# Kernel optimization log

Measured on AMD Instinct MI355X. Metric: run time of the kernel, lower is better.

## Reference

```python
import jax
import jax.numpy as jnp
import numpy as np

VOCAB = 100      # len(vocab); embedding table has VOCAB+1 rows
EMBED = 10
MID = 100
SEQ = 550
OUT = 1


def setup_inputs() -> dict:
    key = jax.random.key(0)
    ks = jax.random.split(key, 8)
    s_ih = 1.0 / np.sqrt(MID)
    return {
        "x": jax.random.randint(ks[0], (SEQ,), 0, VOCAB + 1),
        "hidden": jnp.zeros((1, 1, MID), dtype=jnp.float32),
        "embed_table": jax.random.normal(ks[1], (VOCAB + 1, EMBED), dtype=jnp.float32),
        "w_ih": jax.random.uniform(ks[2], (3 * MID, EMBED), minval=-s_ih, maxval=s_ih, dtype=jnp.float32),
        "w_hh": jax.random.uniform(ks[3], (3 * MID, MID), minval=-s_ih, maxval=s_ih, dtype=jnp.float32),
        "b_ih": jax.random.uniform(ks[4], (3 * MID,), minval=-s_ih, maxval=s_ih, dtype=jnp.float32),
        "b_hh": jax.random.uniform(ks[5], (3 * MID,), minval=-s_ih, maxval=s_ih, dtype=jnp.float32),
        "fc_w": jax.random.uniform(ks[6], (OUT, MID), minval=-s_ih, maxval=s_ih, dtype=jnp.float32),
        "fc_b": jax.random.uniform(ks[7], (OUT,), minval=-s_ih, maxval=s_ih, dtype=jnp.float32),
    }


def reference(x, hidden, embed_table, w_ih, w_hh, b_ih, b_hh, fc_w, fc_b):
    # embedding lookup: [SEQ, EMBED]
    emb = embed_table[x]
    # precompute input-side gate projections for all timesteps: [SEQ, 3*MID]
    gi_all = emb @ w_ih.T + b_ih
    h0 = hidden[0, 0]  # [MID]

    def step(h, gi):
        gh = w_hh @ h + b_hh                      # [3*MID]
        i_r, i_z, i_n = jnp.split(gi, 3)
        h_r, h_z, h_n = jnp.split(gh, 3)
        r = jax.nn.sigmoid(i_r + h_r)
        z = jax.nn.sigmoid(i_z + h_z)
        n = jnp.tanh(i_n + r * h_n)
        h_new = (1.0 - z) * n + z * h
        return h_new, None

    h_final, _ = jax.lax.scan(step, h0, gi_all)   # h_final: [MID]
    out = jax.nn.sigmoid(jax.nn.relu(h_final) @ fc_w.T + fc_b)  # [OUT]
    return out.reshape(1, 1, OUT)
```

## Files before the change

kernel.cpp:

```cpp
#include <hip/hip_runtime.h>

#define SEQ 550
#define MID 100
#define TPB 256

typedef _Float16 half2_t __attribute__((ext_vector_type(2)));

union H2I { int i; half2_t h; ushort2 u2; };

__device__ __forceinline__ float fdot2(half2_t a, half2_t b, float c) {
    return __builtin_amdgcn_fdot2(a, b, c, false);
}
__device__ __forceinline__ float sigm(float x) { return 1.0f / (1.0f + __expf(-x)); }
__device__ __forceinline__ float tanh_f(float x) { return 1.0f - 2.0f / (__expf(2.0f * x) + 1.0f); }
__device__ __forceinline__ half2_t i2h(int v) { H2I u; u.i = v; return u.h; }

__device__ __forceinline__ float pair_sum(float x) {
    int yi = __builtin_amdgcn_update_dpp(0, __float_as_int(x), 0xB1, 0xF, 0xF, true);
    return x + __int_as_float(yi);
}

__global__ __launch_bounds__(TPB, 1) void gru_fused(
    const int*   __restrict__ x,
    const float* __restrict__ hidden,
    const float* __restrict__ embed,
    const float* __restrict__ w_ih,
    const float* __restrict__ w_hh,
    const float* __restrict__ b_ih,
    const float* __restrict__ b_hh,
    const float* __restrict__ fc_w,
    const float* __restrict__ fc_b,
    float*       __restrict__ out)
{
    __shared__ __align__(16) ushort seqbuf[SEQ * 16];
    __shared__ __align__(16) int hbuf[128];
    __shared__ float partial[MID];

    const int  tid = threadIdx.x;
    const bool act = tid < 2 * MID;
    const int  u   = tid >> 1;
    const int  p   = tid & 1;
    const int  hidx = (u < 50) ? u : u + 14;

    for (int i = tid; i < SEQ * 10; i += TPB) {
        int t = i / 10;
        int k = i - 10 * t;
        H2I c; c.h = half2_t{(_Float16)embed[x[t] * 10 + k], (_Float16)0.0f};
        seqbuf[t * 16 + (k < 6 ? k : k + 2)] = c.u2.x;
    }
    for (int i = tid; i < SEQ; i += TPB)
        *(int*)(seqbuf + i * 16 + 12) = 0;

    half2_t whh[3][25];
    half2_t wihr[3][3];
    float b0 = 0.f, b1 = 0.f, b2 = 0.f, b3 = 0.f;
    float hreg = 0.f, fcw = 0.f;

    if (act) {
        #pragma unroll
        for (int r = 0; r < 3; r++) {
            const int row = r * MID + u;
            const float2* wr = (const float2*)(w_hh + row * MID) + 25 * p;
            #pragma unroll
            for (int k = 0; k < 25; k++) {
                float2 f = wr[k];
                whh[r][k] = half2_t{(_Float16)f.x, (_Float16)f.y};
            }
            const float* wi = w_ih + row * 10 + 6 * p;
            wihr[r][0] = half2_t{(_Float16)wi[0], (_Float16)wi[1]};
            wihr[r][1] = half2_t{(_Float16)wi[2], (_Float16)wi[3]};
            if (p == 0) wihr[r][2] = half2_t{(_Float16)wi[4], (_Float16)wi[5]};
            else        wihr[r][2] = half2_t{(_Float16)0.0f, (_Float16)0.0f};
        }
        if (p == 0) {
            b0 = b_ih[u]           + b_hh[u];
            b1 = b_ih[MID + u]     + b_hh[MID + u];
            b2 = b_ih[2 * MID + u];
            b3 = b_hh[2 * MID + u];
        }
        hreg = hidden[u];
        fcw  = fc_w[u];
        if (p == 0) ((_Float16*)hbuf)[hidx] = (_Float16)hreg;
    }
    float fcb = (tid == 0) ? fc_b[0] : 0.0f;

    __syncthreads();

    #pragma unroll 1
    for (int t = 0; t < SEQ; t++) {
        if (act) {
            const int   rbase = ((t & 1) << 8) + (p << 7);
            const int4* hp4   = (const int4*)((const char*)hbuf + rbase);
            int4 q0 = hp4[0], q1 = hp4[1], q2 = hp4[2], q3 = hp4[3], q4 = hp4[4], q5 = hp4[5];
            int  qe = ((const int*)hp4)[24];
            int4 ev = *(const int4*)(seqbuf + t * 16 + p * 8);

            half2_t hh[25];
            hh[0]=i2h(q0.x);  hh[1]=i2h(q0.y);  hh[2]=i2h(q0.z);  hh[3]=i2h(q0.w);
            hh[4]=i2h(q1.x);  hh[5]=i2h(q1.y);  hh[6]=i2h(q1.z);  hh[7]=i2h(q1.w);
            hh[8]=i2h(q2.x);  hh[9]=i2h(q2.y);  hh[10]=i2h(q2.z); hh[11]=i2h(q2.w);
            hh[12]=i2h(q3.x); hh[13]=i2h(q3.y); hh[14]=i2h(q3.z); hh[15]=i2h(q3.w);
            hh[16]=i2h(q4.x); hh[17]=i2h(q4.y); hh[18]=i2h(q4.z); hh[19]=i2h(q4.w);
            hh[20]=i2h(q5.x); hh[21]=i2h(q5.y); hh[22]=i2h(q5.z); hh[23]=i2h(q5.w);
            hh[24]=i2h(qe);

            float s0 = b0, s1 = b1, s2 = b2, s3 = b3;
            #pragma unroll
            for (int k = 0; k < 25; k++) {
                s0 = fdot2(whh[0][k], hh[k], s0);
                s1 = fdot2(whh[1][k], hh[k], s1);
                s3 = fdot2(whh[2][k], hh[k], s3);
            }
            half2_t e0 = i2h(ev.x), e1 = i2h(ev.y), e2 = i2h(ev.z);
            s0 = fdot2(wihr[0][0], e0, s0); s0 = fdot2(wihr[0][1], e1, s0); s0 = fdot2(wihr[0][2], e2, s0);
            s1 = fdot2(wihr[1][0], e0, s1); s1 = fdot2(wihr[1][1], e1, s1); s1 = fdot2(wihr[1][2], e2, s1);
            s2 = fdot2(wihr[2][0], e0, s2); s2 = fdot2(wihr[2][1], e1, s2); s2 = fdot2(wihr[2][2], e2, s2);

            float ar  = pair_sum(s0);
            float az  = pair_sum(s1);
            float gin = pair_sum(s2);
            float ghn = pair_sum(s3);

            float r = sigm(ar);
            float z = sigm(az);
            float n = tanh_f(gin + r * ghn);
            hreg = n + z * (hreg - n);
            if (p == 0)
                ((_Float16*)hbuf)[(((t & 1) ^ 1) << 7) + hidx] = (_Float16)hreg;
        }
        __syncthreads();
    }

    if (act && p == 0) partial[u] = fmaxf(hreg, 0.0f) * fcw;
    __syncthreads();
    if (tid == 0) {
        float s = fcb;
        const float4* pp = (const float4*)partial;
        #pragma unroll
        for (int k = 0; k < 25; k++) {
            float4 f = pp[k];
            s += (f.x + f.y) + (f.z + f.w);
        }
        out[0] = sigm(s);
    }
}

extern "C" void kernel_launch(void* const* d_in, const int* in_sizes, int n_in,
                              void* d_out, int out_size, void* d_ws, size_t ws_size,
                              hipStream_t stream) {
    const int*   x      = (const int*)  d_in[0];
    const float* hidden = (const float*)d_in[1];
    const float* embed  = (const float*)d_in[2];
    const float* w_ih   = (const float*)d_in[3];
    const float* w_hh   = (const float*)d_in[4];
    const float* b_ih   = (const float*)d_in[5];
    const float* b_hh   = (const float*)d_in[6];
    const float* fc_w   = (const float*)d_in[7];
    const float* fc_b   = (const float*)d_in[8];
    float*       out    = (float*)d_out;

    gru_fused<<<1, TPB, 0, stream>>>(x, hidden, embed, w_ih, w_hh,
                                     b_ih, b_hh, fc_w, fc_b, out);
}
```

Measured before the change: 294.7 us.

## Split each GRU unit across four lanes and stage embeddings in hidden buffer

Each hidden unit is now computed by four threads instead of two, so each thread does about 15 fdot2 per gate instead of 28, and the partial sums are combined with a two-step DPP quad reduction. The embedding pair for the next step is copied into the hidden-state buffer by helper threads, so the dot-product loop reads h and x from a single contiguous LDS segment. This shortens the per-step serial dependency chain but adds another DPP stage, more waves taking part in the barrier, and extra helper writes each step.

```diff
diff --git a/kernel.cpp b/kernel.cpp
--- a/kernel.cpp
+++ b/kernel.cpp
@@ -2,7 +2,7 @@
 
 #define SEQ 550
 #define MID 100
-#define TPB 256
+#define TPB 448
 
 typedef _Float16 half2_t __attribute__((ext_vector_type(2)));
 
@@ -15,10 +15,13 @@
 __device__ __forceinline__ float tanh_f(float x) { return 1.0f - 2.0f / (__expf(2.0f * x) + 1.0f); }
 __device__ __forceinline__ half2_t i2h(int v) { H2I u; u.i = v; return u.h; }
 
-__device__ __forceinline__ float pair_sum(float x) {
-    int yi = __builtin_amdgcn_update_dpp(0, __float_as_int(x), 0xB1, 0xF, 0xF, true);
-    return x + __int_as_float(yi);
+__device__ __forceinline__ float qsum(float x) {
+    int a = __builtin_amdgcn_update_dpp(0, __float_as_int(x), 0xB1, 0xF, 0xF, true);
+    float y = x + __int_as_float(a);
+    int b = __builtin_amdgcn_update_dpp(0, __float_as_int(y), 0x4E, 0xF, 0xF, true);
+    return y + __int_as_float(b);
 }
+
 
 __global__ __launch_bounds__(TPB, 1) void gru_fused(
     const int*   __restrict__ x,
@@ -32,45 +35,52 @@
     const float* __restrict__ fc_b,
     float*       __restrict__ out)
 {
-    __shared__ __align__(16) ushort seqbuf[SEQ * 16];
-    __shared__ __align__(16) int hbuf[128];
+    __shared__ __align__(16) int   seqbuf[SEQ * 5];
+    __shared__ __align__(16) int   hbuf[128];
     __shared__ float partial[MID];
 
     const int  tid = threadIdx.x;
-    const bool act = tid < 2 * MID;
-    const int  u   = tid >> 1;
-    const int  p   = tid & 1;
-    const int  hidx = (u < 50) ? u : u + 14;
+    const bool act = tid < 4 * MID;
+    const int  u   = tid >> 2;
+    const int  p   = tid & 3;
 
-    for (int i = tid; i < SEQ * 10; i += TPB) {
-        int t = i / 10;
-        int k = i - 10 * t;
-        H2I c; c.h = half2_t{(_Float16)embed[x[t] * 10 + k], (_Float16)0.0f};
-        seqbuf[t * 16 + (k < 6 ? k : k + 2)] = c.u2.x;
+    if (tid < 128) hbuf[tid] = 0;
+    for (int i = tid; i < SEQ * 5; i += TPB) {
+        int t = i / 5, j = i - 5 * t;
+        const float* ep = embed + x[t] * 10 + 2 * j;
+        H2I c; c.h = half2_t{(_Float16)ep[0], (_Float16)ep[1]};
+        seqbuf[i] = c.i;
     }
-    for (int i = tid; i < SEQ; i += TPB)
-        *(int*)(seqbuf + i * 16 + 12) = 0;
 
-    half2_t whh[3][25];
-    half2_t wihr[3][3];
-    float b0 = 0.f, b1 = 0.f, b2 = 0.f, b3 = 0.f;
-    float hreg = 0.f, fcw = 0.f;
+    half2_t w0[15], w1[15], wn[15];
+    float b0 = 0.f, b1 = 0.f, b2 = 0.f, b3 = 0.f, hreg = 0.f, fcw = 0.f;
+    int hw_off = 0;
 
     if (act) {
+        const int segbase[4] = {0, 13, 26, 38};
+        const int segcnt[4]  = {13, 13, 12, 12};
+        const int ebase[4]   = {0, 2, 3, 4};
+        const int ecnt[4]    = {2, 1, 1, 1};
+
         #pragma unroll
         for (int r = 0; r < 3; r++) {
-            const int row = r * MID + u;
-            const float2* wr = (const float2*)(w_hh + row * MID) + 25 * p;
+            const float* WH = w_hh + (r * MID + u) * MID;
+            const float* WI = w_ih + (r * MID + u) * 10;
+            half2_t* W = (r == 0) ? w0 : (r == 1) ? w1 : wn;
             #pragma unroll
-            for (int k = 0; k < 25; k++) {
-                float2 f = wr[k];
-                whh[r][k] = half2_t{(_Float16)f.x, (_Float16)f.y};
+            for (int pos = 0; pos < 13; pos++) {
+                int m  = segbase[p] + pos;
+                int mc = m < 49 ? m : 49;
+                half2_t wv = half2_t{(_Float16)WH[2 * mc], (_Float16)WH[2 * mc + 1]};
+                W[pos] = (pos < segcnt[p]) ? wv : half2_t{(_Float16)0.f, (_Float16)0.f};
             }
-            const float* wi = w_ih + row * 10 + 6 * p;
-            wihr[r][0] = half2_t{(_Float16)wi[0], (_Float16)wi[1]};
-            wihr[r][1] = half2_t{(_Float16)wi[2], (_Float16)wi[3]};
-            if (p == 0) wihr[r][2] = half2_t{(_Float16)wi[4], (_Float16)wi[5]};
-            else        wihr[r][2] = half2_t{(_Float16)0.0f, (_Float16)0.0f};
+            #pragma unroll
+            for (int j = 0; j < 2; j++) {
+                int m  = ebase[p] + j;
+                int mc = m < 4 ? m : 4;
+                half2_t wv = half2_t{(_Float16)WI[2 * mc], (_Float16)WI[2 * mc + 1]};
+                W[13 + j] = (j < ecnt[p]) ? wv : half2_t{(_Float16)0.f, (_Float16)0.f};
+            }
         }
         if (p == 0) {
             b0 = b_ih[u]           + b_hh[u];
@@ -80,53 +90,64 @@
         }
         hreg = hidden[u];
         fcw  = fc_w[u];
-        if (p == 0) ((_Float16*)hbuf)[hidx] = (_Float16)hreg;
+        int m   = u >> 1;
+        int seg = (m < 13) ? 0 : (m < 26) ? 1 : (m < 38) ? 2 : 3;
+        hw_off  = seg * 64 + (m - segbase[seg]) * 4 + (u & 1) * 2;
     }
     float fcb = (tid == 0) ? fc_b[0] : 0.0f;
 
+    const int he = tid - 400;
+    const int my_eslot = (he == 0) ? 52 : (he == 1) ? 56 :
+                         (he == 2) ? 116 : (he == 3) ? 180 : 244;
+
     __syncthreads();
+
+    if (act && p == 0)
+        *(_Float16*)((char*)hbuf + hw_off) = (_Float16)hreg;
+    if (tid >= 400 && tid < 405)
+        *(int*)((char*)hbuf + my_eslot) = seqbuf[he];
+    __syncthreads();
+
+    const char* rdbase = (const char*)hbuf + p * 64;
 
     #pragma unroll 1
     for (int t = 0; t < SEQ; t++) {
+        const int rpar = (t & 1) << 8;
+        const int wpar = rpar ^ 256;
         if (act) {
-            const int   rbase = ((t & 1) << 8) + (p << 7);
-            const int4* hp4   = (const int4*)((const char*)hbuf + rbase);
-            int4 q0 = hp4[0], q1 = hp4[1], q2 = hp4[2], q3 = hp4[3], q4 = hp4[4], q5 = hp4[5];
-            int  qe = ((const int*)hp4)[24];
-            int4 ev = *(const int4*)(seqbuf + t * 16 + p * 8);
+            const int4* qp = (const int4*)(rdbase + rpar);
+            int4 q0 = qp[0], q1 = qp[1], q2 = qp[2], q3 = qp[3];
+            float s0 = b0, s1 = b1, s2 = b2, s3 = b3;
+            half2_t v;
+            v = i2h(q0.x); s0 = fdot2(w0[0],  v, s0); s1 = fdot2(w1[0],  v, s1); s3 = fdot2(wn[0],  v, s3);
+            v = i2h(q0.y); s0 = fdot2(w0[1],  v, s0); s1 = fdot2(w1[1],  v, s1); s3 = fdot2(wn[1],  v, s3);
+            v = i2h(q0.z); s0 = fdot2(w0[2],  v, s0); s1 = fdot2(w1[2],  v, s1); s3 = fdot2(wn[2],  v, s3);
+            v = i2h(q0.w); s0 = fdot2(w0[3],  v, s0); s1 = fdot2(w1[3],  v, s1); s3 = fdot2(wn[3],  v, s3);
+            v = i2h(q1.x); s0 = fdot2(w0[4],  v, s0); s1 = fdot2(w1[4],  v, s1); s3 = fdot2(wn[4],  v, s3);
+            v = i2h(q1.y); s0 = fdot2(w0[5],  v, s0); s1 = fdot2(w1[5],  v, s1); s3 = fdot2(wn[5],  v, s3);
+            v = i2h(q1.z); s0 = fdot2(w0[6],  v, s0); s1 = fdot2(w1[6],  v, s1); s3 = fdot2(wn[6],  v, s3);
+            v = i2h(q1.w); s0 = fdot2(w0[7],  v, s0); s1 = fdot2(w1[7],  v, s1); s3 = fdot2(wn[7],  v, s3);
+            v = i2h(q2.x); s0 = fdot2(w0[8],  v, s0); s1 = fdot2(w1[8],  v, s1); s3 = fdot2(wn[8],  v, s3);
+            v = i2h(q2.y); s0 = fdot2(w0[9],  v, s0); s1 = fdot2(w1[9],  v, s1); s3 = fdot2(wn[9],  v, s3);
+            v = i2h(q2.z); s0 = fdot2(w0[10], v, s0); s1 = fdot2(w1[10], v, s1); s3 = fdot2(wn[10], v, s3);
+            v = i2h(q2.w); s0 = fdot2(w0[11], v, s0); s1 = fdot2(w1[11], v, s1); s3 = fdot2(wn[11], v, s3);
+            v = i2h(q3.x); s0 = fdot2(w0[12], v, s0); s1 = fdot2(w1[12], v, s1); s3 = fdot2(wn[12], v, s3);
+            v = i2h(q3.y); s0 = fdot2(w0[13], v, s0); s1 = fdot2(w1[13], v, s1); s2 = fdot2(wn[13], v, s2);
+            v = i2h(q3.z); s0 = fdot2(w0[14], v, s0); s1 = fdot2(w1[14], v, s1); s2 = fdot2(wn[14], v, s2);
 
-            half2_t hh[25];
-            hh[0]=i2h(q0.x);  hh[1]=i2h(q0.y);  hh[2]=i2h(q0.z);  hh[3]=i2h(q0.w);
-            hh[4]=i2h(q1.x);  hh[5]=i2h(q1.y);  hh[6]=i2h(q1.z);  hh[7]=i2h(q1.w);
-            hh[8]=i2h(q2.x);  hh[9]=i2h(q2.y);  hh[10]=i2h(q2.z); hh[11]=i2h(q2.w);
-            hh[12]=i2h(q3.x); hh[13]=i2h(q3.y); hh[14]=i2h(q3.z); hh[15]=i2h(q3.w);
-            hh[16]=i2h(q4.x); hh[17]=i2h(q4.y); hh[18]=i2h(q4.z); hh[19]=i2h(q4.w);
-            hh[20]=i2h(q5.x); hh[21]=i2h(q5.y); hh[22]=i2h(q5.z); hh[23]=i2h(q5.w);
-            hh[24]=i2h(qe);
-
-            float s0 = b0, s1 = b1, s2 = b2, s3 = b3;
-            #pragma unroll
-            for (int k = 0; k < 25; k++) {
-                s0 = fdot2(whh[0][k], hh[k], s0);
-                s1 = fdot2(whh[1][k], hh[k], s1);
-                s3 = fdot2(whh[2][k], hh[k], s3);
-            }
-            half2_t e0 = i2h(ev.x), e1 = i2h(ev.y), e2 = i2h(ev.z);
-            s0 = fdot2(wihr[0][0], e0, s0); s0 = fdot2(wihr[0][1], e1, s0); s0 = fdot2(wihr[0][2], e2, s0);
-            s1 = fdot2(wihr[1][0], e0, s1); s1 = fdot2(wihr[1][1], e1, s1); s1 = fdot2(wihr[1][2], e2, s1);
-            s2 = fdot2(wihr[2][0], e0, s2); s2 = fdot2(wihr[2][1], e1, s2); s2 = fdot2(wihr[2][2], e2, s2);
-
-            float ar  = pair_sum(s0);
-            float az  = pair_sum(s1);
-            float gin = pair_sum(s2);
-            float ghn = pair_sum(s3);
+            float ar  = qsum(s0);
+            float az  = qsum(s1);
+            float gin = qsum(s2);
+            float ghn = qsum(s3);
 
             float r = sigm(ar);
             float z = sigm(az);
             float n = tanh_f(gin + r * ghn);
             hreg = n + z * (hreg - n);
             if (p == 0)
-                ((_Float16*)hbuf)[(((t & 1) ^ 1) << 7) + hidx] = (_Float16)hreg;
+                *(_Float16*)((char*)hbuf + wpar + hw_off) = (_Float16)hreg;
+        } else if (tid >= 400 && tid < 405 && t + 1 < SEQ) {
+            *(int*)((char*)hbuf + wpar + my_eslot) = seqbuf[(t + 1) * 5 + he];
         }
         __syncthreads();
     }
```

Result: slower. 357.4 us (+21.3%).

## Run GRU recurrence in a single wavefront using MFMA for hidden-state matvec

Applied to the files above, without the earlier changes.

Moves the recurrent w_hh·h product onto MFMA 16x16x32 f16 instructions issued by one 64-lane wavefront, with weights held as A-fragments in registers. Each lane then finishes two hidden units using fdot2 for the tail columns and input projection. The per-step block-wide __syncthreads is gone because only one wave runs the loop, leaving only intra-wave LDS exchanges. The risks are MFMA latency on the serial dependency chain, heavy register pressure, and relying on intra-wave LDS ordering with no explicit barriers.

```diff
diff --git a/kernel.cpp b/kernel.cpp
--- a/kernel.cpp
+++ b/kernel.cpp
@@ -2,11 +2,14 @@
 
 #define SEQ 550
 #define MID 100
-#define TPB 256
+#define TPB 128
 
 typedef _Float16 half2_t __attribute__((ext_vector_type(2)));
-
-union H2I { int i; half2_t h; ushort2 u2; };
+typedef _Float16 half8_t __attribute__((ext_vector_type(8)));
+typedef float f32x4 __attribute__((ext_vector_type(4)));
+
+union H2I { int i; half2_t h; };
+union H8I { int4 i4; half8_t h8; };
 
 __device__ __forceinline__ float fdot2(half2_t a, half2_t b, float c) {
     return __builtin_amdgcn_fdot2(a, b, c, false);
@@ -14,10 +17,28 @@
 __device__ __forceinline__ float sigm(float x) { return 1.0f / (1.0f + __expf(-x)); }
 __device__ __forceinline__ float tanh_f(float x) { return 1.0f - 2.0f / (__expf(2.0f * x) + 1.0f); }
 __device__ __forceinline__ half2_t i2h(int v) { H2I u; u.i = v; return u.h; }
-
-__device__ __forceinline__ float pair_sum(float x) {
-    int yi = __builtin_amdgcn_update_dpp(0, __float_as_int(x), 0xB1, 0xF, 0xF, true);
-    return x + __int_as_float(yi);
+__device__ __forceinline__ float pull_odd(float x) {
+    int y = __builtin_amdgcn_update_dpp(0, __float_as_int(x), 0xB1, 0xF, 0xF, true);
+    return __int_as_float(y);
+}
+
+template<int BASE, int CNT>
+__device__ __forceinline__ void mfma_group(const half8_t (&afr)[19][3],
+                                           half8_t b0, half8_t b1, half8_t b2,
+                                           f32x4 zf, char* gw, int m) {
+    f32x4 dd[CNT];
+    #pragma unroll
+    for (int j = 0; j < CNT; j++) {
+        f32x4 d = __builtin_amdgcn_mfma_f32_16x16x32_f16(afr[BASE + j][0], b0, zf, 0, 0, 0);
+        d = __builtin_amdgcn_mfma_f32_16x16x32_f16(afr[BASE + j][1], b1, d, 0, 0, 0);
+        d = __builtin_amdgcn_mfma_f32_16x16x32_f16(afr[BASE + j][2], b2, d, 0, 0, 0);
+        dd[j] = d;
+    }
+    if (m == 0) {
+        #pragma unroll
+        for (int j = 0; j < CNT; j++)
+            *(f32x4*)(gw + 64 * (BASE + j)) = dd[j];
+    }
 }
 
 __global__ __launch_bounds__(TPB, 1) void gru_fused(
@@ -32,117 +53,164 @@
     const float* __restrict__ fc_b,
     float*       __restrict__ out)
 {
-    __shared__ __align__(16) ushort seqbuf[SEQ * 16];
-    __shared__ __align__(16) int hbuf[128];
-    __shared__ float partial[MID];
-
-    const int  tid = threadIdx.x;
-    const bool act = tid < 2 * MID;
-    const int  u   = tid >> 1;
-    const int  p   = tid & 1;
-    const int  hidx = (u < 50) ? u : u + 14;
-
-    for (int i = tid; i < SEQ * 10; i += TPB) {
-        int t = i / 10;
-        int k = i - 10 * t;
-        H2I c; c.h = half2_t{(_Float16)embed[x[t] * 10 + k], (_Float16)0.0f};
-        seqbuf[t * 16 + (k < 6 ? k : k + 2)] = c.u2.x;
-    }
-    for (int i = tid; i < SEQ; i += TPB)
-        *(int*)(seqbuf + i * 16 + 12) = 0;
-
-    half2_t whh[3][25];
-    half2_t wihr[3][3];
-    float b0 = 0.f, b1 = 0.f, b2 = 0.f, b3 = 0.f;
-    float hreg = 0.f, fcw = 0.f;
-
-    if (act) {
+    __shared__ __align__(16) int   seqbuf[SEQ * 8];
+    __shared__ __align__(16) int   gates[340];
+    __shared__ __align__(16) int   hbuf[128];
+    __shared__ __align__(16) float partial[64];
+
+    const int tid = threadIdx.x;
+    const int L  = tid & 63;
+    const int m  = L & 15;
+    const int g  = L >> 4;
+    const int L2 = (L < 36) ? L : 35;
+
+    for (int i = tid; i < SEQ * 5; i += TPB) {
+        int t = i / 5, j = i - 5 * t;
+        const float* ep = embed + x[t] * 10 + 2 * j;
+        H2I c; c.h = half2_t{(_Float16)ep[0], (_Float16)ep[1]};
+        seqbuf[t * 8 + j] = c.i;
+    }
+    if (tid < 128) {
+        int v = 0;
+        if (tid < 50) { H2I c; c.h = half2_t{(_Float16)hidden[2 * tid], (_Float16)hidden[2 * tid + 1]}; v = c.i; }
+        hbuf[tid] = v;
+    }
+
+    half8_t afr[19][3];
+    #pragma unroll
+    for (int tt = 0; tt < 19; tt++) {
+        int row = 16 * tt + m;
         #pragma unroll
-        for (int r = 0; r < 3; r++) {
-            const int row = r * MID + u;
-            const float2* wr = (const float2*)(w_hh + row * MID) + 25 * p;
-            #pragma unroll
-            for (int k = 0; k < 25; k++) {
-                float2 f = wr[k];
-                whh[r][k] = half2_t{(_Float16)f.x, (_Float16)f.y};
-            }
-            const float* wi = w_ih + row * 10 + 6 * p;
-            wihr[r][0] = half2_t{(_Float16)wi[0], (_Float16)wi[1]};
-            wihr[r][1] = half2_t{(_Float16)wi[2], (_Float16)wi[3]};
-            if (p == 0) wihr[r][2] = half2_t{(_Float16)wi[4], (_Float16)wi[5]};
-            else        wihr[r][2] = half2_t{(_Float16)0.0f, (_Float16)0.0f};
-        }
-        if (p == 0) {
-            b0 = b_ih[u]           + b_hh[u];
-            b1 = b_ih[MID + u]     + b_hh[MID + u];
-            b2 = b_ih[2 * MID + u];
-            b3 = b_hh[2 * MID + u];
-        }
-        hreg = hidden[u];
-        fcw  = fc_w[u];
-        if (p == 0) ((_Float16*)hbuf)[hidx] = (_Float16)hreg;
-    }
-    float fcb = (tid == 0) ? fc_b[0] : 0.0f;
+        for (int kk = 0; kk < 3; kk++) {
+            half8_t a;
+            if (row < 300) {
+                const float* s = w_hh + row * MID + 32 * kk + 8 * g;
+                float4 f0 = *(const float4*)s;
+                float4 f1 = *(const float4*)(s + 4);
+                a = half8_t{(_Float16)f0.x, (_Float16)f0.y, (_Float16)f0.z, (_Float16)f0.w,
+                            (_Float16)f1.x, (_Float16)f1.y, (_Float16)f1.z, (_Float16)f1.w};
+            } else {
+                a = half8_t{(_Float16)0.f, (_Float16)0.f, (_Float16)0.f, (_Float16)0.f,
+                            (_Float16)0.f, (_Float16)0.f, (_Float16)0.f, (_Float16)0.f};
+            }
+            afr[tt][kk] = a;
+        }
+    }
+
+    half2_t wt[6][7];
+    {
+        const int rowsv[6] = { L, 100 + L, 200 + L, 64 + L2, 164 + L2, 264 + L2 };
+        #pragma unroll
+        for (int rr = 0; rr < 6; rr++) {
+            const float* wh = w_hh + rowsv[rr] * MID + 96;
+            wt[rr][0] = half2_t{(_Float16)wh[0], (_Float16)wh[1]};
+            wt[rr][1] = half2_t{(_Float16)wh[2], (_Float16)wh[3]};
+            const float* wi = w_ih + rowsv[rr] * 10;
+            #pragma unroll
+            for (int k = 0; k < 5; k++)
+                wt[rr][2 + k] = half2_t{(_Float16)wi[2 * k], (_Float16)wi[2 * k + 1]};
+        }
+    }
+    const float bias_r1 = b_ih[L]        + b_hh[L];
+    const float bias_z1 = b_ih[100 + L]  + b_hh[100 + L];
+    const float bias_in1 = b_ih[200 + L];
+    const float bias_hn1 = b_hh[200 + L];
+    const float bias_r2 = b_ih[64 + L2]  + b_hh[64 + L2];
+    const float bias_z2 = b_ih[164 + L2] + b_hh[164 + L2];
+    const float bias_in2 = b_ih[264 + L2];
+    const float bias_hn2 = b_hh[264 + L2];
+
+    float h1  = hidden[L];
+    float h2u = hidden[64 + L2];
+    const float fw1 = fc_w[L];
+    const float fw2 = fc_w[64 + L2];
+
+    char*       gB    = (char*)gates;
+    char*       gw    = gB + 16 * g;
+    const char* gr    = gB + 4 * L;
+    const char* hB    = (const char*)hbuf;
+    const char* bread = hB + 16 * g;
+    const int hw1 = ((L & 1) == 0) ? 2 * L : 256 + 4 * L;
+    const int hw2 = (((L & 1) == 0) && (L < 36)) ? 128 + 2 * L : 256 + 4 * L;
 
     __syncthreads();
 
-    #pragma unroll 1
-    for (int t = 0; t < SEQ; t++) {
-        if (act) {
-            const int   rbase = ((t & 1) << 8) + (p << 7);
-            const int4* hp4   = (const int4*)((const char*)hbuf + rbase);
-            int4 q0 = hp4[0], q1 = hp4[1], q2 = hp4[2], q3 = hp4[3], q4 = hp4[4], q5 = hp4[5];
-            int  qe = ((const int*)hp4)[24];
-            int4 ev = *(const int4*)(seqbuf + t * 16 + p * 8);
-
-            half2_t hh[25];
-            hh[0]=i2h(q0.x);  hh[1]=i2h(q0.y);  hh[2]=i2h(q0.z);  hh[3]=i2h(q0.w);
-            hh[4]=i2h(q1.x);  hh[5]=i2h(q1.y);  hh[6]=i2h(q1.z);  hh[7]=i2h(q1.w);
-            hh[8]=i2h(q2.x);  hh[9]=i2h(q2.y);  hh[10]=i2h(q2.z); hh[11]=i2h(q2.w);
-            hh[12]=i2h(q3.x); hh[13]=i2h(q3.y); hh[14]=i2h(q3.z); hh[15]=i2h(q3.w);
-            hh[16]=i2h(q4.x); hh[17]=i2h(q4.y); hh[18]=i2h(q4.z); hh[19]=i2h(q4.w);
-            hh[20]=i2h(q5.x); hh[21]=i2h(q5.y); hh[22]=i2h(q5.z); hh[23]=i2h(q5.w);
-            hh[24]=i2h(qe);
-
-            float s0 = b0, s1 = b1, s2 = b2, s3 = b3;
-            #pragma unroll
-            for (int k = 0; k < 25; k++) {
-                s0 = fdot2(whh[0][k], hh[k], s0);
-                s1 = fdot2(whh[1][k], hh[k], s1);
-                s3 = fdot2(whh[2][k], hh[k], s3);
-            }
-            half2_t e0 = i2h(ev.x), e1 = i2h(ev.y), e2 = i2h(ev.z);
-            s0 = fdot2(wihr[0][0], e0, s0); s0 = fdot2(wihr[0][1], e1, s0); s0 = fdot2(wihr[0][2], e2, s0);
-            s1 = fdot2(wihr[1][0], e0, s1); s1 = fdot2(wihr[1][1], e1, s1); s1 = fdot2(wihr[1][2], e2, s1);
-            s2 = fdot2(wihr[2][0], e0, s2); s2 = fdot2(wihr[2][1], e1, s2); s2 = fdot2(wihr[2][2], e2, s2);
-
-            float ar  = pair_sum(s0);
-            float az  = pair_sum(s1);
-            float gin = pair_sum(s2);
-            float ghn = pair_sum(s3);
-
-            float r = sigm(ar);
-            float z = sigm(az);
-            float n = tanh_f(gin + r * ghn);
-            hreg = n + z * (hreg - n);
-            if (p == 0)
-                ((_Float16*)hbuf)[(((t & 1) ^ 1) << 7) + hidx] = (_Float16)hreg;
-        }
-        __syncthreads();
-    }
-
-    if (act && p == 0) partial[u] = fmaxf(hreg, 0.0f) * fcw;
+    if (tid < 64) {
+        const f32x4 zf = {0.f, 0.f, 0.f, 0.f};
+        #pragma unroll 1
+        for (int t = 0; t < SEQ; t++) {
+            H8I b0, b1, b2;
+            b0.i4 = *(const int4*)(bread);
+            b1.i4 = *(const int4*)(bread + 64);
+            b2.i4 = *(const int4*)(bread + 128);
+            int2 ht = *(const int2*)(hB + 192);
+            const int* eb = seqbuf + t * 8;
+            int4 e4 = *(const int4*)eb;
+            int  e1 = eb[4];
+            half2_t tv[7] = { i2h(ht.x), i2h(ht.y),
+                              i2h(e4.x), i2h(e4.y), i2h(e4.z), i2h(e4.w), i2h(e1) };
+
+            mfma_group<0, 5>(afr, b0.h8, b1.h8, b2.h8, zf, gw, m);
+            mfma_group<5, 5>(afr, b0.h8, b1.h8, b2.h8, zf, gw, m);
+            mfma_group<10, 5>(afr, b0.h8, b1.h8, b2.h8, zf, gw, m);
+            mfma_group<15, 4>(afr, b0.h8, b1.h8, b2.h8, zf, gw, m);
+
+            float ar1 = bias_r1, az1 = bias_z1, ar2 = bias_r2, az2 = bias_z2;
+            #pragma unroll
+            for (int k = 0; k < 7; k++) {
+                ar1 = fdot2(wt[0][k], tv[k], ar1);
+                az1 = fdot2(wt[1][k], tv[k], az1);
+                ar2 = fdot2(wt[3][k], tv[k], ar2);
+                az2 = fdot2(wt[4][k], tv[k], az2);
+            }
+            float ghn1 = fdot2(wt[2][0], tv[0], bias_hn1); ghn1 = fdot2(wt[2][1], tv[1], ghn1);
+            float ghn2 = fdot2(wt[5][0], tv[0], bias_hn2); ghn2 = fdot2(wt[5][1], tv[1], ghn2);
+            float gin1 = bias_in1, gin2 = bias_in2;
+            #pragma unroll
+            for (int k = 2; k < 7; k++) {
+                gin1 = fdot2(wt[2][k], tv[k], gin1);
+                gin2 = fdot2(wt[5][k], tv[k], gin2);
+            }
+
+            float mr1 = *(const float*)(gr);
+            float mz1 = *(const float*)(gr + 400);
+            float mn1 = *(const float*)(gr + 800);
+            float mr2 = *(const float*)(gr + 256);
+            float mz2 = *(const float*)(gr + 656);
+            float mn2 = *(const float*)(gr + 1056);
+
+            float r1 = sigm(mr1 + ar1);
+            float z1 = sigm(mz1 + az1);
+            float n1 = tanh_f(gin1 + r1 * (mn1 + ghn1));
+            h1 = n1 + z1 * (h1 - n1);
+            float r2 = sigm(mr2 + ar2);
+            float z2 = sigm(mz2 + az2);
+            float n2 = tanh_f(gin2 + r2 * (mn2 + ghn2));
+            h2u = n2 + z2 * (h2u - n2);
+
+            float h1n = pull_odd(h1);
+            H2I p1; p1.h = half2_t{(_Float16)h1, (_Float16)h1n};
+            *(int*)((char*)hbuf + hw1) = p1.i;
+            float h2n = pull_odd(h2u);
+            H2I p2; p2.h = half2_t{(_Float16)h2u, (_Float16)h2n};
+            *(int*)((char*)hbuf + hw2) = p2.i;
+        }
+
+        float acc = fmaxf(h1, 0.f) * fw1;
+        if (L < 36) acc += fmaxf(h2u, 0.f) * fw2;
+        partial[L] = acc;
+        if (L == 0) {
+            float s = fc_b[0];
+            const float4* pp = (const float4*)partial;
+            #pragma unroll
+            for (int k = 0; k < 16; k++) {
+                float4 f = pp[k];
+                s += (f.x + f.y) + (f.z + f.w);
+            }
+            out[0] = sigm(s);
+        }
+    }
     __syncthreads();
-    if (tid == 0) {
-        float s = fcb;
-        const float4* pp = (const float4*)partial;
-        #pragma unroll
-        for (int k = 0; k < 25; k++) {
-            float4 f = pp[k];
-            s += (f.x + f.y) + (f.z + f.w);
-        }
-        out[0] = sigm(s);
-    }
 }
 
 extern "C" void kernel_launch(void* const* d_in, const int* in_sizes, int n_in,
```

New measurement: 686.1 us. 2.33x slower.

## Compute GRU recurrent matvec with MFMA 16x16x32 across two waves

Applied to the files above, without the earlier changes.

Replaces the per-thread fdot2 recurrent matvec (two threads per hidden unit, 200 active threads) with MFMA f16 instructions over 128 threads: each wave owns 50 hidden units, and each MFMA tile covers 4 units times 3 gates. The first 96 hidden columns go through 39 chained MFMAs per step. The remaining 4 columns and the input projection are handled with fdot2, which removes the DPP pair reduction. The aim is fewer threads and barrier participants and less VALU work per step, at the cost of a serial MFMA dependency chain and select-based extraction of the results on the latency-bound recurrence.

```diff
diff --git a/kernel.cpp b/kernel.cpp
--- a/kernel.cpp
+++ b/kernel.cpp
@@ -2,11 +2,14 @@
 
 #define SEQ 550
 #define MID 100
-#define TPB 256
+#define TPB 128
 
 typedef _Float16 half2_t __attribute__((ext_vector_type(2)));
+typedef _Float16 half8_t __attribute__((ext_vector_type(8)));
+typedef float f32x4 __attribute__((ext_vector_type(4)));
 
-union H2I { int i; half2_t h; ushort2 u2; };
+union H2I { int i; half2_t h; };
+union H8I { int4 i4; half8_t h8; };
 
 __device__ __forceinline__ float fdot2(half2_t a, half2_t b, float c) {
     return __builtin_amdgcn_fdot2(a, b, c, false);
@@ -15,10 +18,6 @@
 __device__ __forceinline__ float tanh_f(float x) { return 1.0f - 2.0f / (__expf(2.0f * x) + 1.0f); }
 __device__ __forceinline__ half2_t i2h(int v) { H2I u; u.i = v; return u.h; }
 
-__device__ __forceinline__ float pair_sum(float x) {
-    int yi = __builtin_amdgcn_update_dpp(0, __float_as_int(x), 0xB1, 0xF, 0xF, true);
-    return x + __int_as_float(yi);
-}
 
 __global__ __launch_bounds__(TPB, 1) void gru_fused(
     const int*   __restrict__ x,
@@ -32,106 +31,136 @@
     const float* __restrict__ fc_b,
     float*       __restrict__ out)
 {
-    __shared__ __align__(16) ushort seqbuf[SEQ * 16];
-    __shared__ __align__(16) int hbuf[128];
+    __shared__ __align__(16) int  seqbuf[SEQ * 8];
+    __shared__ __align__(16) char hlds[512];
     __shared__ float partial[MID];
 
-    const int  tid = threadIdx.x;
-    const bool act = tid < 2 * MID;
-    const int  u   = tid >> 1;
-    const int  p   = tid & 1;
-    const int  hidx = (u < 50) ? u : u + 14;
+    const int tid = threadIdx.x;
+    const int w   = tid >> 6;
+    const int l   = tid & 63;
+    const int m   = l & 15;
+    const int g   = l >> 4;
+    const int qg  = m >> 2;
+    const int rt  = m & 3;
 
-    for (int i = tid; i < SEQ * 10; i += TPB) {
-        int t = i / 10;
-        int k = i - 10 * t;
-        H2I c; c.h = half2_t{(_Float16)embed[x[t] * 10 + k], (_Float16)0.0f};
-        seqbuf[t * 16 + (k < 6 ? k : k + 2)] = c.u2.x;
+    for (int i = tid; i < SEQ * 5; i += TPB) {
+        int t = i / 5, j = i - 5 * t;
+        const float* ep = embed + x[t] * 10 + 2 * j;
+        H2I c; c.h = half2_t{(_Float16)ep[0], (_Float16)ep[1]};
+        seqbuf[t * 8 + j] = c.i;
     }
-    for (int i = tid; i < SEQ; i += TPB)
-        *(int*)(seqbuf + i * 16 + 12) = 0;
 
-    half2_t whh[3][25];
-    half2_t wihr[3][3];
-    float b0 = 0.f, b1 = 0.f, b2 = 0.f, b3 = 0.f;
-    float hreg = 0.f, fcw = 0.f;
+    half8_t afr[13][3];
+    #pragma unroll
+    for (int t = 0; t < 13; t++) {
+        int j = 13 * qg + t;
+        bool av = (rt < 3) && (j < 50);
+        int wrow = rt * MID + 50 * w + (j < 50 ? j : 0);
+        #pragma unroll
+        for (int kk = 0; kk < 3; kk++) {
+            half8_t a = half8_t{(_Float16)0.f, (_Float16)0.f, (_Float16)0.f, (_Float16)0.f,
+                                (_Float16)0.f, (_Float16)0.f, (_Float16)0.f, (_Float16)0.f};
+            if (av) {
+                const float* s = w_hh + wrow * MID + 32 * kk + 8 * g;
+                float4 f0 = *(const float4*)s;
+                float4 f1 = *(const float4*)(s + 4);
+                a = half8_t{(_Float16)f0.x, (_Float16)f0.y, (_Float16)f0.z, (_Float16)f0.w,
+                            (_Float16)f1.x, (_Float16)f1.y, (_Float16)f1.z, (_Float16)f1.w};
+            }
+            afr[t][kk] = a;
+        }
+    }
 
-    if (act) {
+    const int  jm    = 13 * g + m;
+    const bool ismix = (m < 13) && (jm < 50);
+    const int  um    = 50 * w + (jm < 50 ? jm : 0);
+
+    half2_t wtr[7], wtz[7], wtn[7];
+    {
+        const float* hr = w_hh + um * MID + 96;
+        const float* hz = w_hh + (MID + um) * MID + 96;
+        const float* hn = w_hh + (2 * MID + um) * MID + 96;
+        wtr[0] = half2_t{(_Float16)hr[0], (_Float16)hr[1]};
+        wtr[1] = half2_t{(_Float16)hr[2], (_Float16)hr[3]};
+        wtz[0] = half2_t{(_Float16)hz[0], (_Float16)hz[1]};
+        wtz[1] = half2_t{(_Float16)hz[2], (_Float16)hz[3]};
+        wtn[0] = half2_t{(_Float16)hn[0], (_Float16)hn[1]};
+        wtn[1] = half2_t{(_Float16)hn[2], (_Float16)hn[3]};
+        const float* ir = w_ih + um * 10;
+        const float* iz = w_ih + (MID + um) * 10;
+        const float* in_ = w_ih + (2 * MID + um) * 10;
         #pragma unroll
-        for (int r = 0; r < 3; r++) {
-            const int row = r * MID + u;
-            const float2* wr = (const float2*)(w_hh + row * MID) + 25 * p;
-            #pragma unroll
-            for (int k = 0; k < 25; k++) {
-                float2 f = wr[k];
-                whh[r][k] = half2_t{(_Float16)f.x, (_Float16)f.y};
-            }
-            const float* wi = w_ih + row * 10 + 6 * p;
-            wihr[r][0] = half2_t{(_Float16)wi[0], (_Float16)wi[1]};
-            wihr[r][1] = half2_t{(_Float16)wi[2], (_Float16)wi[3]};
-            if (p == 0) wihr[r][2] = half2_t{(_Float16)wi[4], (_Float16)wi[5]};
-            else        wihr[r][2] = half2_t{(_Float16)0.0f, (_Float16)0.0f};
+        for (int k = 0; k < 5; k++) {
+            wtr[2 + k] = half2_t{(_Float16)ir[2 * k], (_Float16)ir[2 * k + 1]};
+            wtz[2 + k] = half2_t{(_Float16)iz[2 * k], (_Float16)iz[2 * k + 1]};
+            wtn[2 + k] = half2_t{(_Float16)in_[2 * k], (_Float16)in_[2 * k + 1]};
         }
-        if (p == 0) {
-            b0 = b_ih[u]           + b_hh[u];
-            b1 = b_ih[MID + u]     + b_hh[MID + u];
-            b2 = b_ih[2 * MID + u];
-            b3 = b_hh[2 * MID + u];
-        }
-        hreg = hidden[u];
-        fcw  = fc_w[u];
-        if (p == 0) ((_Float16*)hbuf)[hidx] = (_Float16)hreg;
     }
-    float fcb = (tid == 0) ? fc_b[0] : 0.0f;
+    const float br  = b_ih[um]           + b_hh[um];
+    const float bz  = b_ih[MID + um]     + b_hh[MID + um];
+    const float bin = b_ih[2 * MID + um];
+    const float bhn = b_hh[2 * MID + um];
+
+    float hreg = hidden[um];
+    const float fcw = fc_w[um];
+    const float fcb = (tid == 0) ? fc_b[0] : 0.0f;
+
+    if (ismix) *(_Float16*)(hlds + 2 * um) = (_Float16)hreg;
 
     __syncthreads();
 
     #pragma unroll 1
     for (int t = 0; t < SEQ; t++) {
-        if (act) {
-            const int   rbase = ((t & 1) << 8) + (p << 7);
-            const int4* hp4   = (const int4*)((const char*)hbuf + rbase);
-            int4 q0 = hp4[0], q1 = hp4[1], q2 = hp4[2], q3 = hp4[3], q4 = hp4[4], q5 = hp4[5];
-            int  qe = ((const int*)hp4)[24];
-            int4 ev = *(const int4*)(seqbuf + t * 16 + p * 8);
+        const char* rb = hlds + ((t & 1) << 8);
+        H8I b0, b1, b2;
+        b0.i4 = *(const int4*)(rb + 16 * g);
+        b1.i4 = *(const int4*)(rb + 64 + 16 * g);
+        b2.i4 = *(const int4*)(rb + 128 + 16 * g);
+        int2 ht = *(const int2*)(rb + 192);
+        const int* eb = seqbuf + t * 8;
+        int4 e4 = *(const int4*)eb;
+        int  e1 = eb[4];
+        half2_t tv0 = i2h(ht.x), tv1 = i2h(ht.y);
+        half2_t tv2 = i2h(e4.x), tv3 = i2h(e4.y), tv4 = i2h(e4.z), tv5 = i2h(e4.w), tv6 = i2h(e1);
 
-            half2_t hh[25];
-            hh[0]=i2h(q0.x);  hh[1]=i2h(q0.y);  hh[2]=i2h(q0.z);  hh[3]=i2h(q0.w);
-            hh[4]=i2h(q1.x);  hh[5]=i2h(q1.y);  hh[6]=i2h(q1.z);  hh[7]=i2h(q1.w);
-            hh[8]=i2h(q2.x);  hh[9]=i2h(q2.y);  hh[10]=i2h(q2.z); hh[11]=i2h(q2.w);
-            hh[12]=i2h(q3.x); hh[13]=i2h(q3.y); hh[14]=i2h(q3.z); hh[15]=i2h(q3.w);
-            hh[16]=i2h(q4.x); hh[17]=i2h(q4.y); hh[18]=i2h(q4.z); hh[19]=i2h(q4.w);
-            hh[20]=i2h(q5.x); hh[21]=i2h(q5.y); hh[22]=i2h(q5.z); hh[23]=i2h(q5.w);
-            hh[24]=i2h(qe);
+        const f32x4 zf = {0.f, 0.f, 0.f, 0.f};
+        float sr = 0.f, sz = 0.f, sn = 0.f;
+        #pragma unroll
+        for (int tt = 0; tt < 13; tt++) {
+            f32x4 d = __builtin_amdgcn_mfma_f32_16x16x32_f16(afr[tt][0], b0.h8, zf, 0, 0, 0);
+            d = __builtin_amdgcn_mfma_f32_16x16x32_f16(afr[tt][1], b1.h8, d, 0, 0, 0);
+            d = __builtin_amdgcn_mfma_f32_16x16x32_f16(afr[tt][2], b2.h8, d, 0, 0, 0);
+            bool c = (m == tt);
+            sr = c ? d[0] : sr;
+            sz = c ? d[1] : sz;
+            sn = c ? d[2] : sn;
+        }
 
-            float s0 = b0, s1 = b1, s2 = b2, s3 = b3;
-            #pragma unroll
-            for (int k = 0; k < 25; k++) {
-                s0 = fdot2(whh[0][k], hh[k], s0);
-                s1 = fdot2(whh[1][k], hh[k], s1);
-                s3 = fdot2(whh[2][k], hh[k], s3);
-            }
-            half2_t e0 = i2h(ev.x), e1 = i2h(ev.y), e2 = i2h(ev.z);
-            s0 = fdot2(wihr[0][0], e0, s0); s0 = fdot2(wihr[0][1], e1, s0); s0 = fdot2(wihr[0][2], e2, s0);
-            s1 = fdot2(wihr[1][0], e0, s1); s1 = fdot2(wihr[1][1], e1, s1); s1 = fdot2(wihr[1][2], e2, s1);
-            s2 = fdot2(wihr[2][0], e0, s2); s2 = fdot2(wihr[2][1], e1, s2); s2 = fdot2(wihr[2][2], e2, s2);
+        float ar = br, az = bz, gin = bin, ghn = bhn;
+        ar = fdot2(wtr[0], tv0, ar); ar = fdot2(wtr[1], tv1, ar);
+        ar = fdot2(wtr[2], tv2, ar); ar = fdot2(wtr[3], tv3, ar);
+        ar = fdot2(wtr[4], tv4, ar); ar = fdot2(wtr[5], tv5, ar);
+        ar = fdot2(wtr[6], tv6, ar);
+        az = fdot2(wtz[0], tv0, az); az = fdot2(wtz[1], tv1, az);
+        az = fdot2(wtz[2], tv2, az); az = fdot2(wtz[3], tv3, az);
+        az = fdot2(wtz[4], tv4, az); az = fdot2(wtz[5], tv5, az);
+        az = fdot2(wtz[6], tv6, az);
+        ghn = fdot2(wtn[0], tv0, ghn); ghn = fdot2(wtn[1], tv1, ghn);
+        gin = fdot2(wtn[2], tv2, gin); gin = fdot2(wtn[3], tv3, gin);
+        gin = fdot2(wtn[4], tv4, gin); gin = fdot2(wtn[5], tv5, gin);
+        gin = fdot2(wtn[6], tv6, gin);
 
-            float ar  = pair_sum(s0);
-            float az  = pair_sum(s1);
-            float gin = pair_sum(s2);
-            float ghn = pair_sum(s3);
+        float r = sigm(sr + ar);
+        float z = sigm(sz + az);
+        float n = tanh_f(gin + r * (sn + ghn));
+        hreg = n + z * (hreg - n);
+        if (ismix)
+            *(_Float16*)(hlds + (((t & 1) ^ 1) << 8) + 2 * um) = (_Float16)hreg;
 
-            float r = sigm(ar);
-            float z = sigm(az);
-            float n = tanh_f(gin + r * ghn);
-            hreg = n + z * (hreg - n);
-            if (p == 0)
-                ((_Float16*)hbuf)[(((t & 1) ^ 1) << 7) + hidx] = (_Float16)hreg;
-        }
         __syncthreads();
     }
 
-    if (act && p == 0) partial[u] = fmaxf(hreg, 0.0f) * fcw;
+    if (ismix) partial[um] = fmaxf(hreg, 0.f) * fcw;
     __syncthreads();
     if (tid == 0) {
         float s = fcb;
```

After: 418.6 us. +42.0%, slower.
